# Optimization experiments

Hardware: AMD Instinct MI355X
Metric: run time of the kernel (lower is better)

## Reference

```python
import jax, jax.numpy as jnp
import numpy as np

OUT, IN, RANK = 4096, 4096, 512
B, S = 4, 2048


def setup_inputs() -> dict:
    key = jax.random.key(0)
    k_x, k_qa, k_qb, k_sa, k_sb, k_b = jax.random.split(key, 6)
    x = jax.random.normal(k_x, (B, S, IN), dtype=jnp.float32)
    # int8-style symmetric quantized CP factors (stored as int32 for the harness)
    q_a = jax.random.randint(k_qa, (OUT, RANK), -127, 127, dtype=jnp.int32)
    q_b = jax.random.randint(k_qb, (IN, RANK), -127, 127, dtype=jnp.int32)
    scale_a = jax.random.uniform(k_sa, (), dtype=jnp.float32) * 0.01 + 1e-4
    scale_b = jax.random.uniform(k_sb, (), dtype=jnp.float32) * 0.01 + 1e-4
    bias = jax.random.normal(k_b, (OUT,), dtype=jnp.float32)
    return {"x": x, "q_a": q_a, "q_b": q_b, "scale_a": scale_a,
            "scale_b": scale_b, "bias": bias}


def reference(x, q_a, q_b, scale_a, scale_b, bias):
    # dequantize_factors(): symmetric per-factor dequant q * scale
    a = q_a.astype(jnp.float32) * scale_a          # [OUT, RANK]
    b = q_b.astype(jnp.float32) * scale_b          # [IN,  RANK]
    # CP reconstruction: weight = factors[0] @ factors[1].T, viewed as [OUT, IN]
    weight = a @ b.T                               # [OUT, IN] (materialized, as in original)
    # F.linear(x, weight, bias) = x @ weight.T + bias
    return jnp.einsum('bsi,oi->bso', x, weight) + bias
```

## Files before the change

### kernel.cpp

```cpp
#include <hip/hip_runtime.h>
#include <hip/hip_fp16.h>


#define M_TOT 8192
#define N_OUT 4096
#define K_IN  4096
#define RANK  512

typedef _Float16 f16x8 __attribute__((ext_vector_type(8)));
typedef float f32x4 __attribute__((ext_vector_type(4)));

#define WAIT_VM0() asm volatile("s_waitcnt vmcnt(0)" ::: "memory")
#define BARRIER() do { __builtin_amdgcn_s_barrier(); __builtin_amdgcn_sched_barrier(0); } while (0)

__device__ __forceinline__ void gload_lds16(const void* g, void* l) {
  __builtin_amdgcn_global_load_lds(
      (const __attribute__((address_space(1))) unsigned int*)g,
      (__attribute__((address_space(3))) unsigned int*)l, 16, 0, 0);
}

__global__ void k_cvt_qa(const int4* __restrict__ q, ushort4* __restrict__ o, int n4) {
  int i = blockIdx.x * blockDim.x + threadIdx.x;
  if (i >= n4) return;
  int4 v = q[i];
  ushort4 r;
  r.x = __half_as_ushort(__float2half_rn((float)v.x));
  r.y = __half_as_ushort(__float2half_rn((float)v.y));
  r.z = __half_as_ushort(__float2half_rn((float)v.z));
  r.w = __half_as_ushort(__float2half_rn((float)v.w));
  o[i] = r;
}

__global__ void k_transpose_qb(const int* __restrict__ qb, __half* __restrict__ qbt) {
  __shared__ __half tile[32][33];
  int tx = threadIdx.x & 31, ty = threadIdx.x >> 5;
  int k0 = blockIdx.x * 32, r0 = blockIdx.y * 32;
#pragma unroll
  for (int j = 0; j < 4; ++j)
    tile[ty + j * 8][tx] = __float2half_rn((float)qb[(size_t)(k0 + ty + j * 8) * RANK + r0 + tx]);
  __syncthreads();
#pragma unroll
  for (int j = 0; j < 4; ++j)
    qbt[(size_t)(r0 + ty + j * 8) * K_IN + k0 + tx] = tile[tx][ty + j * 8];
}

__global__ __launch_bounds__(512, 2) void k_gemm1v(
    const float* __restrict__ X, const __half* __restrict__ Bt,
    __half* __restrict__ P) {
  __shared__ __align__(16) uint4 lds[2][2048];
  const int tid = threadIdx.x;
  const int lane = tid & 63, wid = tid >> 6;
  const int wm = wid & 1, wn = wid >> 1;
  const int blk = blockIdx.x;
  const int xcd = blk & 7, m_t = blk >> 3;
  const int z = xcd >> 1, n_t = xcd & 1;
  const int m0 = m_t * 128, n0 = n_t * 256;
  const int kbeg = z * (K_IN / 4);
  const int fr = lane & 15, fq = lane >> 4;

  f32x4 acc[4][4] = {};

  auto stage = [&](int kt, int buf) {
#pragma unroll
    for (int c = 0; c < 2; ++c) {
      int d = tid + 512 * c;
      int r = d >> 3, s = (d & 7) ^ (r & 7);
      gload_lds16(X + (size_t)(m0 + r) * K_IN + kbeg + kt * 32 + s * 4, &lds[buf][d]);
    }
#pragma unroll
    for (int c = 0; c < 2; ++c) {
      int d = tid + 512 * c;
      int p = d >> 3, u = (d & 7) ^ (p & 7);
      gload_lds16(Bt + (size_t)(n0 + 2 * p + (u >> 2)) * K_IN + kbeg + kt * 32 + (u & 3) * 8,
                  &lds[buf][1024 + d]);
    }
  };

  stage(0, 0);
  WAIT_VM0();
  BARRIER();

  const int NT = (K_IN / 4) / 32;
  for (int t = 0; t < NT; ++t) {
    if (t + 1 < NT) stage(t + 1, (t + 1) & 1);
    const uint4* Ab = &lds[t & 1][0];
    const uint4* Bb = &lds[t & 1][1024];
    f16x8 a[4], b[4];
#pragma unroll
    for (int mi = 0; mi < 4; ++mi) {
      int r = wm * 64 + mi * 16 + fr;
      f32x4 u0 = *(const f32x4*)&Ab[r * 8 + ((fq * 2) ^ (r & 7))];
      f32x4 u1 = *(const f32x4*)&Ab[r * 8 + ((fq * 2 + 1) ^ (r & 7))];
      union { __half2 h[4]; f16x8 v; } pa;
      pa.h[0] = __floats2half2_rn(u0[0], u0[1]);
      pa.h[1] = __floats2half2_rn(u0[2], u0[3]);
      pa.h[2] = __floats2half2_rn(u1[0], u1[1]);
      pa.h[3] = __floats2half2_rn(u1[2], u1[3]);
      a[mi] = pa.v;
    }
#pragma unroll
    for (int ni = 0; ni < 4; ++ni) {
      int r = wn * 64 + ni * 16 + fr;
      int p = r >> 1;
      b[ni] = *(const f16x8*)&Bb[p * 8 + ((((r & 1) << 2) | fq) ^ (p & 7))];
    }
#pragma unroll
    for (int mi = 0; mi < 4; ++mi)
#pragma unroll
      for (int ni = 0; ni < 4; ++ni)
        acc[mi][ni] = __builtin_amdgcn_mfma_f32_16x16x32_f16(a[mi], b[ni], acc[mi][ni], 0, 0, 0);

    if (t + 1 < NT) WAIT_VM0();
    BARRIER();
  }

  __half* Pz = P + (size_t)z * M_TOT * RANK;
#pragma unroll
  for (int mi = 0; mi < 4; ++mi)
#pragma unroll
    for (int ni = 0; ni < 4; ++ni) {
      int col = n0 + wn * 64 + ni * 16 + fr;
      int rbase = m0 + wm * 64 + mi * 16 + fq * 4;
#pragma unroll
      for (int j = 0; j < 4; ++j)
        Pz[(size_t)(rbase + j) * RANK + col] = __float2half_rn(acc[mi][ni][j]);
    }
}

__global__ void k_reduce_t(const uint4* __restrict__ P, uint4* __restrict__ T8, int n8) {
  int i = blockIdx.x * blockDim.x + threadIdx.x;
  if (i >= n8) return;
  float2 f[4] = {};
#pragma unroll
  for (int zz = 0; zz < 4; ++zz) {
    uint4 v = P[(size_t)zz * n8 + i];
    const __half2* h = (const __half2*)&v;
#pragma unroll
    for (int j = 0; j < 4; ++j) {
      float2 g = __half22float2(h[j]);
      f[j].x += g.x; f[j].y += g.y;
    }
  }
  uint4 r;
  __half2* o = (__half2*)&r;
#pragma unroll
  for (int j = 0; j < 4; ++j) o[j] = __floats2half2_rn(f[j].x, f[j].y);
  T8[i] = r;
}

__global__ __launch_bounds__(256, 2) void k_gemm2(
    const __half* __restrict__ T, const __half* __restrict__ QA,
    const float* __restrict__ sa, const float* __restrict__ sb,
    const float* __restrict__ bias, float* __restrict__ Out) {
  __shared__ __align__(16) uint4 lds[2][2048];
  const int tid = threadIdx.x;
  const int lane = tid & 63, wid = tid >> 6, wm = wid & 1, wn = wid >> 1;
  const int flat = blockIdx.x;
  const int xcd = flat & 7, local = flat >> 3;
  const int n_t = xcd * 4 + (local & 3);
  const int m_t = local >> 2;
  const int m0 = m_t * 128, n0 = n_t * 128;
  const int fr = lane & 15, fq = lane >> 4;

  f32x4 acc[4][4] = {};

  auto stage = [&](int kt, int buf) {
#pragma unroll
    for (int c = 0; c < 4; ++c) {
      int d = tid + 256 * c;
      int r = d >> 3, s = (d & 7) ^ (r & 7);
      gload_lds16(T + (size_t)(m0 + r) * RANK + kt * 64 + s * 8, &lds[buf][d]);
    }
#pragma unroll
    for (int c = 0; c < 4; ++c) {
      int d = tid + 256 * c;
      int r = d >> 3, s = (d & 7) ^ (r & 7);
      gload_lds16(QA + (size_t)(n0 + r) * RANK + kt * 64 + s * 8, &lds[buf][1024 + d]);
    }
  };

  stage(0, 0);
  WAIT_VM0();
  BARRIER();

  const int NT = RANK / 64;
  for (int t = 0; t < NT; ++t) {
    if (t + 1 < NT) stage(t + 1, (t + 1) & 1);
    const int cur = t & 1;
#pragma unroll
    for (int kk = 0; kk < 2; ++kk) {
      int s = kk * 4 + fq;
      f16x8 a[4], b[4];
#pragma unroll
      for (int mi = 0; mi < 4; ++mi) {
        int r = wm * 64 + mi * 16 + fr;
        a[mi] = *(const f16x8*)&lds[cur][r * 8 + (s ^ (r & 7))];
      }
#pragma unroll
      for (int ni = 0; ni < 4; ++ni) {
        int n = wn * 64 + ni * 16 + fr;
        b[ni] = *(const f16x8*)&lds[cur][1024 + n * 8 + (s ^ (n & 7))];
      }
#pragma unroll
      for (int mi = 0; mi < 4; ++mi)
#pragma unroll
        for (int ni = 0; ni < 4; ++ni)
          acc[mi][ni] = __builtin_amdgcn_mfma_f32_16x16x32_f16(a[mi], b[ni], acc[mi][ni], 0, 0, 0);
    }
    if (t + 1 < NT) WAIT_VM0();
    BARRIER();
  }

  const float scale = sa[0] * sb[0];
#pragma unroll
  for (int mi = 0; mi < 4; ++mi)
#pragma unroll
    for (int ni = 0; ni < 4; ++ni) {
      int col = n0 + wn * 64 + ni * 16 + fr;
      float bv = bias[col];
      int rbase = m0 + wm * 64 + mi * 16 + fq * 4;
#pragma unroll
      for (int j = 0; j < 4; ++j)
        Out[(size_t)(rbase + j) * N_OUT + col] = acc[mi][ni][j] * scale + bv;
    }
}

extern "C" void kernel_launch(void* const* d_in, const int* in_sizes, int n_in,
                              void* d_out, int out_size, void* d_ws, size_t ws_size,
                              hipStream_t stream) {
  const float* x    = (const float*)d_in[0];
  const int*   qa   = (const int*)d_in[1];
  const int*   qb   = (const int*)d_in[2];
  const float* sa   = (const float*)d_in[3];
  const float* sb   = (const float*)d_in[4];
  const float* bias = (const float*)d_in[5];
  float* out = (float*)d_out;

  char* ws = (char*)d_ws;
  __half* qa_h = (__half*)ws;
  __half* qbt  = (__half*)(ws + (4u << 20));
  __half* t    = (__half*)(ws + (8u << 20));
  __half* part = (__half*)(ws + (16u << 20));

  k_cvt_qa<<<2048, 256, 0, stream>>>((const int4*)qa, (ushort4*)qa_h, (N_OUT * RANK) / 4);
  dim3 tg(K_IN / 32, RANK / 32);
  k_transpose_qb<<<tg, 256, 0, stream>>>(qb, qbt);

  k_gemm1v<<<512, 512, 0, stream>>>(x, qbt, part);

  const int n8 = M_TOT * RANK / 8;
  k_reduce_t<<<n8 / 256, 256, 0, stream>>>((const uint4*)part, (uint4*)t, n8);

  k_gemm2<<<2048, 256, 0, stream>>>(t, qa_h, sa, sb, bias, out);
}
```

Measured before the change: 149.4 us.

## Prefetch two stages ahead in both GEMMs and fuse qa conversion into reduce

Both GEMM main loops now issue loads two K-tiles ahead with partial vmcnt waits, so global-to-LDS copies overlap more compute. The price is an extra barrier per iteration, needed to protect buffer reuse. The qa int-to-half conversion kernel is merged into the partial-sum reduce kernel, which removes one launch. k_gemm1v's launch bounds are raised to 4 blocks per SM, which may constrain registers and cause spills.

```diff
diff --git a/kernel.cpp b/kernel.cpp
--- a/kernel.cpp
+++ b/kernel.cpp
@@ -11,6 +11,8 @@
 typedef float f32x4 __attribute__((ext_vector_type(4)));
 
 #define WAIT_VM0() asm volatile("s_waitcnt vmcnt(0)" ::: "memory")
+#define WAIT_VM4() asm volatile("s_waitcnt vmcnt(4)" ::: "memory")
+#define WAIT_VM8() asm volatile("s_waitcnt vmcnt(8)" ::: "memory")
 #define BARRIER() do { __builtin_amdgcn_s_barrier(); __builtin_amdgcn_sched_barrier(0); } while (0)
 
 __device__ __forceinline__ void gload_lds16(const void* g, void* l) {
@@ -19,18 +21,6 @@
       (__attribute__((address_space(3))) unsigned int*)l, 16, 0, 0);
 }
 
-__global__ void k_cvt_qa(const int4* __restrict__ q, ushort4* __restrict__ o, int n4) {
-  int i = blockIdx.x * blockDim.x + threadIdx.x;
-  if (i >= n4) return;
-  int4 v = q[i];
-  ushort4 r;
-  r.x = __half_as_ushort(__float2half_rn((float)v.x));
-  r.y = __half_as_ushort(__float2half_rn((float)v.y));
-  r.z = __half_as_ushort(__float2half_rn((float)v.z));
-  r.w = __half_as_ushort(__float2half_rn((float)v.w));
-  o[i] = r;
-}
-
 __global__ void k_transpose_qb(const int* __restrict__ qb, __half* __restrict__ qbt) {
   __shared__ __half tile[32][33];
   int tx = threadIdx.x & 31, ty = threadIdx.x >> 5;
@@ -44,7 +34,7 @@
     qbt[(size_t)(r0 + ty + j * 8) * K_IN + k0 + tx] = tile[tx][ty + j * 8];
 }
 
-__global__ __launch_bounds__(512, 2) void k_gemm1v(
+__global__ __launch_bounds__(512, 4) void k_gemm1v(
     const float* __restrict__ X, const __half* __restrict__ Bt,
     __half* __restrict__ P) {
   __shared__ __align__(16) uint4 lds[2][2048];
@@ -77,12 +67,12 @@
   };
 
   stage(0, 0);
-  WAIT_VM0();
+  stage(1, 1);
+  WAIT_VM4();
   BARRIER();
 
   const int NT = (K_IN / 4) / 32;
   for (int t = 0; t < NT; ++t) {
-    if (t + 1 < NT) stage(t + 1, (t + 1) & 1);
     const uint4* Ab = &lds[t & 1][0];
     const uint4* Bb = &lds[t & 1][1024];
     f16x8 a[4], b[4];
@@ -110,7 +100,14 @@
       for (int ni = 0; ni < 4; ++ni)
         acc[mi][ni] = __builtin_amdgcn_mfma_f32_16x16x32_f16(a[mi], b[ni], acc[mi][ni], 0, 0, 0);
 
-    if (t + 1 < NT) WAIT_VM0();
+    if (t == NT - 1) break;
+    BARRIER();
+    if (t + 2 < NT) {
+      stage(t + 2, t & 1);
+      WAIT_VM4();
+    } else {
+      WAIT_VM0();
+    }
     BARRIER();
   }
 
@@ -127,25 +124,39 @@
     }
 }
 
-__global__ void k_reduce_t(const uint4* __restrict__ P, uint4* __restrict__ T8, int n8) {
-  int i = blockIdx.x * blockDim.x + threadIdx.x;
-  if (i >= n8) return;
-  float2 f[4] = {};
-#pragma unroll
-  for (int zz = 0; zz < 4; ++zz) {
-    uint4 v = P[(size_t)zz * n8 + i];
-    const __half2* h = (const __half2*)&v;
-#pragma unroll
-    for (int j = 0; j < 4; ++j) {
-      float2 g = __half22float2(h[j]);
-      f[j].x += g.x; f[j].y += g.y;
-    }
+__global__ void k_reduce_cvt(const uint4* __restrict__ P, uint4* __restrict__ T8, int n8,
+                             const int4* __restrict__ qa, ushort4* __restrict__ qh, int nq4) {
+  int b = blockIdx.x;
+  int nred = n8 / 256;
+  if (b < nred) {
+    int i = b * 256 + threadIdx.x;
+    float2 f[4] = {};
+#pragma unroll
+    for (int zz = 0; zz < 4; ++zz) {
+      uint4 v = P[(size_t)zz * n8 + i];
+      const __half2* h = (const __half2*)&v;
+#pragma unroll
+      for (int j = 0; j < 4; ++j) {
+        float2 g = __half22float2(h[j]);
+        f[j].x += g.x; f[j].y += g.y;
+      }
+    }
+    uint4 r;
+    __half2* o = (__half2*)&r;
+#pragma unroll
+    for (int j = 0; j < 4; ++j) o[j] = __floats2half2_rn(f[j].x, f[j].y);
+    T8[i] = r;
+  } else {
+    int i = (b - nred) * 256 + threadIdx.x;
+    if (i >= nq4) return;
+    int4 v = qa[i];
+    ushort4 r;
+    r.x = __half_as_ushort(__float2half_rn((float)v.x));
+    r.y = __half_as_ushort(__float2half_rn((float)v.y));
+    r.z = __half_as_ushort(__float2half_rn((float)v.z));
+    r.w = __half_as_ushort(__float2half_rn((float)v.w));
+    qh[i] = r;
   }
-  uint4 r;
-  __half2* o = (__half2*)&r;
-#pragma unroll
-  for (int j = 0; j < 4; ++j) o[j] = __floats2half2_rn(f[j].x, f[j].y);
-  T8[i] = r;
 }
 
 __global__ __launch_bounds__(256, 2) void k_gemm2(
@@ -180,12 +191,12 @@
   };
 
   stage(0, 0);
-  WAIT_VM0();
+  stage(1, 1);
+  WAIT_VM8();
   BARRIER();
 
   const int NT = RANK / 64;
   for (int t = 0; t < NT; ++t) {
-    if (t + 1 < NT) stage(t + 1, (t + 1) & 1);
     const int cur = t & 1;
 #pragma unroll
     for (int kk = 0; kk < 2; ++kk) {
@@ -207,7 +218,14 @@
         for (int ni = 0; ni < 4; ++ni)
           acc[mi][ni] = __builtin_amdgcn_mfma_f32_16x16x32_f16(a[mi], b[ni], acc[mi][ni], 0, 0, 0);
     }
-    if (t + 1 < NT) WAIT_VM0();
+    if (t == NT - 1) break;
+    BARRIER();
+    if (t + 2 < NT) {
+      stage(t + 2, cur);
+      WAIT_VM8();
+    } else {
+      WAIT_VM0();
+    }
     BARRIER();
   }
 
@@ -242,14 +260,17 @@
   __half* t    = (__half*)(ws + (8u << 20));
   __half* part = (__half*)(ws + (16u << 20));
 
-  k_cvt_qa<<<2048, 256, 0, stream>>>((const int4*)qa, (ushort4*)qa_h, (N_OUT * RANK) / 4);
   dim3 tg(K_IN / 32, RANK / 32);
   k_transpose_qb<<<tg, 256, 0, stream>>>(qb, qbt);
 
   k_gemm1v<<<512, 512, 0, stream>>>(x, qbt, part);
 
   const int n8 = M_TOT * RANK / 8;
-  k_reduce_t<<<n8 / 256, 256, 0, stream>>>((const uint4*)part, (uint4*)t, n8);
+  const int nq4 = N_OUT * RANK / 4;
+  const int nred = n8 / 256;
+  const int ncvt = (nq4 + 255) / 256;
+  k_reduce_cvt<<<nred + ncvt, 256, 0, stream>>>((const uint4*)part, (uint4*)t, n8,
+                                                (const int4*)qa, (ushort4*)qa_h, nq4);
 
   k_gemm2<<<2048, 256, 0, stream>>>(t, qa_h, sa, sb, bias, out);
 }
```

New measurement: 132.3 us (median of 2 runs). 11.4% less time.
